# Kernel optimization log

Measured on AMD Instinct MI355X. Metric: run time of the kernel, lower is better.

## Reference

```python
import jax, jax.numpy as jnp
import numpy as np

IN_FEATURES = 4096
OUT_FEATURES = 1024
BATCH = 16384
WERR = 1.0
BERR = 1.0


def setup_inputs() -> dict:
    key = jax.random.key(0)
    kx, kw = jax.random.split(key)
    X = jax.random.normal(kx, (BATCH, IN_FEATURES), dtype=jnp.float32)
    # glorot_uniform init for W, zeros for bias (as in Keras layer)
    limit = np.sqrt(6.0 / (IN_FEATURES + OUT_FEATURES)).astype(np.float32)
    W = jax.random.uniform(kw, (IN_FEATURES, OUT_FEATURES), dtype=jnp.float32,
                           minval=-limit, maxval=limit)
    bias = jnp.zeros((1, OUT_FEATURES), dtype=jnp.float32)
    return {"X": X, "W": W, "bias": bias}


def reference(X, W, bias):
    # Binarize weights/bias with sign(), scaled by Werr/Berr, then dense matmul.
    Wb = jnp.sign(W) * WERR          # [in, out], values in {-1, 0, +1}
    bb = jnp.sign(bias) * BERR       # [1, out]
    Z = jnp.matmul(X, Wb) + bb       # [batch, out]
    return Z
```

## Files before the change

### kernel.cpp

```cpp
#include <hip/hip_runtime.h>

#define M_DIM 16384
#define N_DIM 1024
#define K_DIM 4096

#define BM 256
#define BN 256
#define BK 64
#define NT (K_DIM / BK)

typedef __attribute__((ext_vector_type(4))) float f32x4;
typedef __attribute__((ext_vector_type(8))) short bf16x8;
typedef __attribute__((ext_vector_type(8))) unsigned short u16x8;

static __device__ __forceinline__ short f2bf(float f) {
  union { __bf16 h; short s; } u;
  u.h = (__bf16)f;
  return u.s;
}

static __device__ __forceinline__ void load_lds16(const void* g, void* l) {
  __builtin_amdgcn_global_load_lds(
      (const __attribute__((address_space(1))) void*)g,
      (__attribute__((address_space(3))) void*)l, 16, 0, 0);
}

__global__ __launch_bounds__(256) void wsign_transpose(
    const float* __restrict__ W, unsigned short* __restrict__ WbT) {
  __shared__ unsigned short tile[64][72];
  const int t  = (int)threadIdx.x;
  const int k0 = (int)(blockIdx.x >> 4) * 64;
  const int n0 = (int)(blockIdx.x & 15) * 64;
#pragma unroll
  for (int p = 0; p < 4; ++p) {
    const int r = p * 16 + (t >> 4);
    const int c = (t & 15) * 4;
    const float* src = W + (size_t)(k0 + r) * N_DIM + n0 + c;
#pragma unroll
    for (int j = 0; j < 4; ++j) {
      const float w = src[j];
      tile[r][c + j] = (w > 0.f) ? (unsigned short)0x3F80u
                                 : ((w < 0.f) ? (unsigned short)0xBF80u
                                              : (unsigned short)0u);
    }
  }
  __syncthreads();
  const int n  = t >> 2;
  const int kg = (t & 3) * 16;
  u16x8 o0, o1;
#pragma unroll
  for (int j = 0; j < 8; ++j) o0[j] = tile[kg + j][n];
#pragma unroll
  for (int j = 0; j < 8; ++j) o1[j] = tile[kg + 8 + j][n];
  unsigned short* dst = WbT + (size_t)(n0 + n) * K_DIM + k0 + kg;
  *(u16x8*)dst       = o0;
  *(u16x8*)(dst + 8) = o1;
}

__global__ __launch_bounds__(512, 2) void gemm_kk(
    const float* __restrict__ X, const unsigned short* __restrict__ WbT,
    const float* __restrict__ bias, float* __restrict__ Z) {
  __shared__ __align__(16) unsigned short As[2][BM * BK];
  __shared__ __align__(16) unsigned short Bs[2][BN * BK];

  const int t   = (int)threadIdx.x;
  const int l   = t & 63;
  const int wid = t >> 6;
  const int wm  = wid >> 2;
  const int wn  = wid & 3;

  const int bid = (int)blockIdx.x;
  const int swz = (bid & 7) * 32 + (bid >> 3);
  const int m0  = (swz >> 2) * BM;
  const int n0  = (swz & 3) * BN;

  const int abase = (wm * 128 + (l & 15)) * BK;
  const int bbase = (wn * 64 + (l & 15)) * BK;
  const int axk0  = (((l >> 4) + 0) ^ (l & 7)) << 3;
  const int axk1  = (((l >> 4) + 4) ^ (l & 7)) << 3;

  const float* sA0 = X + (size_t)(m0 +   0 + (t >> 3)) * K_DIM + (t & 7) * 8;
  const float* sA1 = X + (size_t)(m0 +  64 + (t >> 3)) * K_DIM + (t & 7) * 8;
  const float* sA2 = X + (size_t)(m0 + 128 + (t >> 3)) * K_DIM + (t & 7) * 8;
  const float* sA3 = X + (size_t)(m0 + 192 + (t >> 3)) * K_DIM + (t & 7) * 8;
  const int adst = (t >> 3) * BK + (((t & 7) ^ ((t >> 3) & 7)) << 3);

  const unsigned short* b_src[4];
  int b_dst[4];
#pragma unroll
  for (int i = 0; i < 4; ++i) {
    const int c = i * 512 + t;
    const int n = c >> 3, gp = c & 7;
    b_src[i] = WbT + (size_t)(n0 + n) * K_DIM + (gp ^ (n & 7)) * 8;
    b_dst[i] = c * 8;
  }

  f32x4 acc[8][4] = {};
  f32x4 ar[4][2];
  bf16x8 aR[4];
  bf16x8 bR[4];

#define SB0 __builtin_amdgcn_sched_barrier(0)
#define BAR do { SB0; __builtin_amdgcn_s_barrier(); SB0; } while (0)
#define WVM(N) do { asm volatile("s_waitcnt vmcnt(" #N ")" ::: "memory"); SB0; } while (0)
#define WLG0 do { asm volatile("s_waitcnt lgkmcnt(0)" ::: "memory"); SB0; } while (0)

#define LD_A8(KT)                                                          \
  do { SB0;                                                                \
    ar[0][0] = *(const f32x4*)(sA0 + (KT));                                \
    ar[0][1] = *(const f32x4*)(sA0 + (KT) + 4);                            \
    ar[1][0] = *(const f32x4*)(sA1 + (KT));                                \
    ar[1][1] = *(const f32x4*)(sA1 + (KT) + 4);                            \
    ar[2][0] = *(const f32x4*)(sA2 + (KT));                                \
    ar[2][1] = *(const f32x4*)(sA2 + (KT) + 4);                            \
    ar[3][0] = *(const f32x4*)(sA3 + (KT));                                \
    ar[3][1] = *(const f32x4*)(sA3 + (KT) + 4); SB0;                       \
  } while (0)
#define WR_AH(BUF, H)                                                      \
  do {                                                                     \
    _Pragma("unroll") for (int j = 2 * (H); j < 2 * (H) + 2; ++j) {        \
      u16x8 v;                                                             \
      _Pragma("unroll") for (int q = 0; q < 4; ++q) {                      \
        v[q]     = (unsigned short)f2bf(ar[j][0][q]);                      \
        v[4 + q] = (unsigned short)f2bf(ar[j][1][q]);                      \
      }                                                                    \
      *(u16x8*)(&As[BUF][adst + j * 4096]) = v;                            \
    }                                                                      \
  } while (0)
#define DMA_B2(KT, BUF, I0)                                                \
  do { SB0;                                                                \
    _Pragma("unroll") for (int i = (I0); i < (I0) + 2; ++i)                \
      load_lds16(b_src[i] + (KT), &Bs[BUF][b_dst[i]]);                     \
    SB0;                                                                   \
  } while (0)
#define RD_A4(KK, MIG, AB)                                                 \
  do { SB0;                                                                \
    _Pragma("unroll") for (int mi = 0; mi < 4; ++mi)                       \
      aR[mi] = *(const bf16x8*)((AB) + abase + ((MIG)*4 + mi) * 1024 +     \
                                ((KK) ? axk1 : axk0));                     \
    SB0;                                                                   \
  } while (0)
#define RD_B4(KK, BB)                                                      \
  do { SB0;                                                                \
    _Pragma("unroll") for (int nj = 0; nj < 4; ++nj)                       \
      bR[nj] = *(const bf16x8*)((BB) + bbase + nj * 1024 +                 \
                                ((KK) ? axk1 : axk0));                     \
    SB0;                                                                   \
  } while (0)
#define MFMA16(MIG)                                                        \
  do { __builtin_amdgcn_s_setprio(1);                                      \
    _Pragma("unroll") for (int mi = 0; mi < 4; ++mi)                       \
      _Pragma("unroll") for (int nj = 0; nj < 4; ++nj)                     \
        acc[(MIG)*4 + mi][nj] = __builtin_amdgcn_mfma_f32_16x16x32_bf16(   \
            aR[mi], bR[nj], acc[(MIG)*4 + mi][nj], 0, 0, 0);               \
    __builtin_amdgcn_s_setprio(0);                                         \
  } while (0)

  LD_A8(0);
  WVM(0);
  WR_AH(0, 0); WR_AH(0, 1);
  DMA_B2(0, 0, 0); DMA_B2(0, 0, 2);
  LD_A8(BK);
  WVM(8);
  WLG0;
  BAR;

  for (int tt = 0; tt <= NT - 3; ++tt) {
    const int cur = tt & 1, nxt = cur ^ 1;
    const unsigned short* Ab = As[cur];
    const unsigned short* Bb = Bs[cur];
    const int kt1 = (tt + 1) * BK, kt2 = (tt + 2) * BK;
    RD_B4(0, Bb);
    RD_A4(0, 0, Ab);
    DMA_B2(kt1, nxt, 0);
    BAR; WLG0;
    MFMA16(0);
    BAR;
    RD_A4(0, 1, Ab);
    DMA_B2(kt1, nxt, 2);
    WVM(4);
    WR_AH(nxt, 0);
    BAR; WLG0;
    MFMA16(1);
    BAR;
    RD_B4(1, Bb);
    RD_A4(1, 0, Ab);
    WR_AH(nxt, 1);
    LD_A8(kt2);
    BAR; WLG0;
    MFMA16(0);
    BAR;
    RD_A4(1, 1, Ab);
    WVM(8);
    BAR; WLG0;
    MFMA16(1);
    BAR;
  }

  {
    const int cur = (NT - 2) & 1, nxt = cur ^ 1;
    const unsigned short* Ab = As[cur];
    const unsigned short* Bb = Bs[cur];
    const int kt1 = (NT - 1) * BK;
    RD_B4(0, Bb);
    RD_A4(0, 0, Ab);
    DMA_B2(kt1, nxt, 0);
    BAR; WLG0;
    MFMA16(0);
    BAR;
    RD_A4(0, 1, Ab);
    DMA_B2(kt1, nxt, 2);
    WVM(4);
    WR_AH(nxt, 0);
    BAR; WLG0;
    MFMA16(1);
    BAR;
    RD_B4(1, Bb);
    RD_A4(1, 0, Ab);
    WR_AH(nxt, 1);
    BAR; WLG0;
    MFMA16(0);
    BAR;
    RD_A4(1, 1, Ab);
    WVM(0);
    BAR; WLG0;
    MFMA16(1);
    BAR;
  }
  {
    const unsigned short* Ab = As[(NT - 1) & 1];
    const unsigned short* Bb = Bs[(NT - 1) & 1];
    RD_B4(0, Bb);
    RD_A4(0, 0, Ab);
    WLG0;
    MFMA16(0);
    RD_A4(0, 1, Ab);
    WLG0;
    MFMA16(1);
    RD_B4(1, Bb);
    RD_A4(1, 0, Ab);
    WLG0;
    MFMA16(0);
    RD_A4(1, 1, Ab);
    WLG0;
    MFMA16(1);
  }

#pragma unroll
  for (int ni = 0; ni < 4; ++ni) {
    const int col = n0 + wn * 64 + ni * 16 + (l & 15);
    const float b  = bias[col];
    const float bs = (b > 0.f) ? 1.f : ((b < 0.f) ? -1.f : 0.f);
#pragma unroll
    for (int mi = 0; mi < 8; ++mi) {
      const int row = m0 + wm * 128 + mi * 16 + ((l >> 4) << 2);
#pragma unroll
      for (int j = 0; j < 4; ++j)
        Z[(size_t)(row + j) * N_DIM + col] = acc[mi][ni][j] + bs;
    }
  }
#undef SB0
#undef BAR
#undef WVM
#undef WLG0
#undef LD_A8
#undef WR_AH
#undef DMA_B2
#undef RD_A4
#undef RD_B4
#undef MFMA16
}

__global__ __launch_bounds__(256) void naive_fb(
    const float* __restrict__ X, const float* __restrict__ W,
    const float* __restrict__ bias, float* __restrict__ Z) {
  const size_t id = (size_t)blockIdx.x * 256 + threadIdx.x;
  const int m = (int)(id >> 10), n = (int)(id & 1023);
  float acc = 0.f;
  for (int k = 0; k < K_DIM; ++k) {
    const float w = W[(size_t)k * N_DIM + n];
    const float s = (w > 0.f) ? 1.f : ((w < 0.f) ? -1.f : 0.f);
    acc += X[(size_t)m * K_DIM + k] * s;
  }
  const float b = bias[n];
  Z[id] = acc + ((b > 0.f) ? 1.f : ((b < 0.f) ? -1.f : 0.f));
}

extern "C" void kernel_launch(void* const* d_in, const int* in_sizes, int n_in,
                              void* d_out, int out_size, void* d_ws, size_t ws_size,
                              hipStream_t stream) {
  const float* X    = (const float*)d_in[0];
  const float* W    = (const float*)d_in[1];
  const float* bias = (const float*)d_in[2];
  float* Z = (float*)d_out;

  const size_t needW = (size_t)N_DIM * K_DIM * sizeof(unsigned short);
  if (ws_size >= needW) {
    unsigned short* WbT = (unsigned short*)d_ws;
    wsign_transpose<<<dim3((K_DIM / 64) * (N_DIM / 64)), dim3(256), 0, stream>>>(W, WbT);
    gemm_kk<<<dim3((M_DIM / BM) * (N_DIM / BN)), dim3(512), 0, stream>>>(X, WbT, bias, Z);
  } else {
    naive_fb<<<dim3((size_t)M_DIM * N_DIM / 256), dim3(256), 0, stream>>>(X, W, bias, Z);
  }
}
```

Baseline: 177.6 us.

## Double-buffer MFMA register fragments and drop most per-phase barriers in GEMM loop

Rewrites the GEMM main loop to keep two sets of A/B register fragments, so LDS reads for the next MFMA phase overlap with the current phase. Each iteration now uses two workgroup barriers instead of eight, with partial lgkmcnt waits in place of full drains. The four B DMA loads per tile are issued together. Separately, the transpose kernel's LDS tile padding changes to reduce bank conflicts. The cost is more registers and hand-counted wait counts, which could cause races or stalls if any count is wrong.

```diff
diff --git a/kernel.cpp b/kernel.cpp
--- a/kernel.cpp
+++ b/kernel.cpp
@@ -27,7 +27,7 @@
 
 __global__ __launch_bounds__(256) void wsign_transpose(
     const float* __restrict__ W, unsigned short* __restrict__ WbT) {
-  __shared__ unsigned short tile[64][72];
+  __shared__ unsigned short tile[64][67];
   const int t  = (int)threadIdx.x;
   const int k0 = (int)(blockIdx.x >> 4) * 64;
   const int n0 = (int)(blockIdx.x & 15) * 64;
@@ -57,7 +57,7 @@
   *(u16x8*)(dst + 8) = o1;
 }
 
-__global__ __launch_bounds__(512, 2) void gemm_kk(
+__global__ __launch_bounds__(512, 2) void gemm_pipe(
     const float* __restrict__ X, const unsigned short* __restrict__ WbT,
     const float* __restrict__ bias, float* __restrict__ Z) {
   __shared__ __align__(16) unsigned short As[2][BM * BK];
@@ -97,13 +97,13 @@
 
   f32x4 acc[8][4] = {};
   f32x4 ar[4][2];
-  bf16x8 aR[4];
-  bf16x8 bR[4];
+  bf16x8 a0F[4], a1F[4];
+  bf16x8 b0F[4], b1F[4];
 
 #define SB0 __builtin_amdgcn_sched_barrier(0)
 #define BAR do { SB0; __builtin_amdgcn_s_barrier(); SB0; } while (0)
 #define WVM(N) do { asm volatile("s_waitcnt vmcnt(" #N ")" ::: "memory"); SB0; } while (0)
-#define WLG0 do { asm volatile("s_waitcnt lgkmcnt(0)" ::: "memory"); SB0; } while (0)
+#define WLG(N) do { asm volatile("s_waitcnt lgkmcnt(" #N ")" ::: "memory"); SB0; } while (0)
 
 #define LD_A8(KT)                                                          \
   do { SB0;                                                                \
@@ -117,7 +117,7 @@
     ar[3][1] = *(const f32x4*)(sA3 + (KT) + 4); SB0;                       \
   } while (0)
 #define WR_AH(BUF, H)                                                      \
-  do {                                                                     \
+  do { SB0;                                                                \
     _Pragma("unroll") for (int j = 2 * (H); j < 2 * (H) + 2; ++j) {        \
       u16x8 v;                                                             \
       _Pragma("unroll") for (int q = 0; q < 4; ++q) {                      \
@@ -125,75 +125,73 @@
         v[4 + q] = (unsigned short)f2bf(ar[j][1][q]);                      \
       }                                                                    \
       *(u16x8*)(&As[BUF][adst + j * 4096]) = v;                            \
-    }                                                                      \
-  } while (0)
-#define DMA_B2(KT, BUF, I0)                                                \
-  do { SB0;                                                                \
-    _Pragma("unroll") for (int i = (I0); i < (I0) + 2; ++i)                \
+    } SB0;                                                                 \
+  } while (0)
+#define DMA_B4(KT, BUF)                                                    \
+  do { SB0;                                                                \
+    _Pragma("unroll") for (int i = 0; i < 4; ++i)                          \
       load_lds16(b_src[i] + (KT), &Bs[BUF][b_dst[i]]);                     \
     SB0;                                                                   \
   } while (0)
-#define RD_A4(KK, MIG, AB)                                                 \
+#define RD_A(DST, KK, MIG, AB)                                             \
   do { SB0;                                                                \
     _Pragma("unroll") for (int mi = 0; mi < 4; ++mi)                       \
-      aR[mi] = *(const bf16x8*)((AB) + abase + ((MIG)*4 + mi) * 1024 +     \
-                                ((KK) ? axk1 : axk0));                     \
+      DST[mi] = *(const bf16x8*)((AB) + abase + ((MIG)*4 + mi) * 1024 +    \
+                                 ((KK) ? axk1 : axk0));                    \
     SB0;                                                                   \
   } while (0)
-#define RD_B4(KK, BB)                                                      \
+#define RD_B(DST, KK, BB)                                                  \
   do { SB0;                                                                \
     _Pragma("unroll") for (int nj = 0; nj < 4; ++nj)                       \
-      bR[nj] = *(const bf16x8*)((BB) + bbase + nj * 1024 +                 \
-                                ((KK) ? axk1 : axk0));                     \
+      DST[nj] = *(const bf16x8*)((BB) + bbase + nj * 1024 +                \
+                                 ((KK) ? axk1 : axk0));                    \
     SB0;                                                                   \
   } while (0)
-#define MFMA16(MIG)                                                        \
+#define MFMA16(MIG, AF, BF)                                                \
   do { __builtin_amdgcn_s_setprio(1);                                      \
     _Pragma("unroll") for (int mi = 0; mi < 4; ++mi)                       \
       _Pragma("unroll") for (int nj = 0; nj < 4; ++nj)                     \
         acc[(MIG)*4 + mi][nj] = __builtin_amdgcn_mfma_f32_16x16x32_bf16(   \
-            aR[mi], bR[nj], acc[(MIG)*4 + mi][nj], 0, 0, 0);               \
+            AF[mi], BF[nj], acc[(MIG)*4 + mi][nj], 0, 0, 0);               \
     __builtin_amdgcn_s_setprio(0);                                         \
   } while (0)
 
   LD_A8(0);
   WVM(0);
   WR_AH(0, 0); WR_AH(0, 1);
-  DMA_B2(0, 0, 0); DMA_B2(0, 0, 2);
+  DMA_B4(0, 0);
   LD_A8(BK);
   WVM(8);
-  WLG0;
+  WLG(0);
   BAR;
+  RD_A(a0F, 0, 0, As[0]);
+  RD_B(b0F, 0, Bs[0]);
 
   for (int tt = 0; tt <= NT - 3; ++tt) {
     const int cur = tt & 1, nxt = cur ^ 1;
     const unsigned short* Ab = As[cur];
     const unsigned short* Bb = Bs[cur];
-    const int kt1 = (tt + 1) * BK, kt2 = (tt + 2) * BK;
-    RD_B4(0, Bb);
-    RD_A4(0, 0, Ab);
-    DMA_B2(kt1, nxt, 0);
-    BAR; WLG0;
-    MFMA16(0);
-    BAR;
-    RD_A4(0, 1, Ab);
-    DMA_B2(kt1, nxt, 2);
+    RD_A(a1F, 0, 1, Ab);
+    DMA_B4((tt + 1) * BK, nxt);
+    WLG(4);
+    MFMA16(0, a0F, b0F);
+    RD_A(a0F, 1, 0, Ab);
+    RD_B(b1F, 1, Bb);
     WVM(4);
     WR_AH(nxt, 0);
-    BAR; WLG0;
-    MFMA16(1);
-    BAR;
-    RD_B4(1, Bb);
-    RD_A4(1, 0, Ab);
+    WLG(10);
+    MFMA16(1, a1F, b0F);
     WR_AH(nxt, 1);
-    LD_A8(kt2);
-    BAR; WLG0;
-    MFMA16(0);
-    BAR;
-    RD_A4(1, 1, Ab);
+    RD_A(a1F, 1, 1, Ab);
+    LD_A8((tt + 2) * BK);
     WVM(8);
-    BAR; WLG0;
-    MFMA16(1);
+    WLG(4);
+    MFMA16(0, a0F, b1F);
+    BAR;
+    RD_A(a0F, 0, 0, As[nxt]);
+    RD_B(b0F, 0, Bs[nxt]);
+    WLG(8);
+    MFMA16(1, a1F, b1F);
     BAR;
   }
 
@@ -201,49 +199,43 @@
     const int cur = (NT - 2) & 1, nxt = cur ^ 1;
     const unsigned short* Ab = As[cur];
     const unsigned short* Bb = Bs[cur];
-    const int kt1 = (NT - 1) * BK;
-    RD_B4(0, Bb);
-    RD_A4(0, 0, Ab);
-    DMA_B2(kt1, nxt, 0);
-    BAR; WLG0;
-    MFMA16(0);
-    BAR;
-    RD_A4(0, 1, Ab);
-    DMA_B2(kt1, nxt, 2);
+    RD_A(a1F, 0, 1, Ab);
+    DMA_B4((NT - 1) * BK, nxt);
+    WLG(4);
+    MFMA16(0, a0F, b0F);
+    RD_A(a0F, 1, 0, Ab);
+    RD_B(b1F, 1, Bb);
     WVM(4);
     WR_AH(nxt, 0);
-    BAR; WLG0;
-    MFMA16(1);
-    BAR;
-    RD_B4(1, Bb);
-    RD_A4(1, 0, Ab);
+    WLG(10);
+    MFMA16(1, a1F, b0F);
     WR_AH(nxt, 1);
-    BAR; WLG0;
-    MFMA16(0);
-    BAR;
-    RD_A4(1, 1, Ab);
+    RD_A(a1F, 1, 1, Ab);
     WVM(0);
-    BAR; WLG0;
-    MFMA16(1);
+    WLG(4);
+    MFMA16(0, a0F, b1F);
+    BAR;
+    RD_A(a0F, 0, 0, As[nxt]);
+    RD_B(b0F, 0, Bs[nxt]);
+    WLG(8);
+    MFMA16(1, a1F, b1F);
     BAR;
   }
   {
     const unsigned short* Ab = As[(NT - 1) & 1];
     const unsigned short* Bb = Bs[(NT - 1) & 1];
-    RD_B4(0, Bb);
-    RD_A4(0, 0, Ab);
-    WLG0;
-    MFMA16(0);
-    RD_A4(0, 1, Ab);
-    WLG0;
-    MFMA16(1);
-    RD_B4(1, Bb);
-    RD_A4(1, 0, Ab);
-    WLG0;
-    MFMA16(0);
-    RD_A4(1, 1, Ab);
-    WLG0;
-    MFMA16(1);
+    RD_A(a1F, 0, 1, Ab);
+    WLG(4);
+    MFMA16(0, a0F, b0F);
+    RD_A(a0F, 1, 0, Ab);
+    RD_B(b1F, 1, Bb);
+    WLG(8);
+    MFMA16(1, a1F, b0F);
+    RD_A(a1F, 1, 1, Ab);
+    WLG(4);
+    MFMA16(0, a0F, b1F);
+    WLG(0);
+    MFMA16(1, a1F, b1F);
   }
 
 #pragma unroll
@@ -262,12 +254,12 @@
 #undef SB0
 #undef BAR
 #undef WVM
-#undef WLG0
+#undef WLG
 #undef LD_A8
 #undef WR_AH
-#undef DMA_B2
-#undef RD_A4
-#undef RD_B4
+#undef DMA_B4
+#undef RD_A
+#undef RD_B
 #undef MFMA16
 }
 
@@ -298,7 +290,7 @@
   if (ws_size >= needW) {
     unsigned short* WbT = (unsigned short*)d_ws;
     wsign_transpose<<<dim3((K_DIM / 64) * (N_DIM / 64)), dim3(256), 0, stream>>>(W, WbT);
-    gemm_kk<<<dim3((M_DIM / BM) * (N_DIM / BN)), dim3(512), 0, stream>>>(X, WbT, bias, Z);
+    gemm_pipe<<<dim3((M_DIM / BM) * (N_DIM / BN)), dim3(512), 0, stream>>>(X, WbT, bias, Z);
   } else {
     naive_fb<<<dim3((size_t)M_DIM * N_DIM / 256), dim3(256), 0, stream>>>(X, W, bias, Z);
   }
```

Result: faster. 172.2 us (-3.1%).

## Load B fragments directly from global into registers, dropping B LDS staging

Applied to the files above, without the earlier changes.

The GEMM no longer stages the binarized weight tile through LDS with global_load_lds. Each wave now loads its B MFMA fragments straight from global memory into registers, double-buffered across k-halves, which halves LDS usage and removes the B LDS reads. The cost is more redundant global/L2 traffic, since waves sharing a column block each reload B, plus more VGPR pressure from two B register sets. The transpose tile padding also changes from 72 to 67 columns.

```diff
diff --git a/kernel.cpp b/kernel.cpp
--- a/kernel.cpp
+++ b/kernel.cpp
@@ -19,15 +19,9 @@
   return u.s;
 }
 
-static __device__ __forceinline__ void load_lds16(const void* g, void* l) {
-  __builtin_amdgcn_global_load_lds(
-      (const __attribute__((address_space(1))) void*)g,
-      (__attribute__((address_space(3))) void*)l, 16, 0, 0);
-}
-
 __global__ __launch_bounds__(256) void wsign_transpose(
     const float* __restrict__ W, unsigned short* __restrict__ WbT) {
-  __shared__ unsigned short tile[64][72];
+  __shared__ unsigned short tile[64][67];
   const int t  = (int)threadIdx.x;
   const int k0 = (int)(blockIdx.x >> 4) * 64;
   const int n0 = (int)(blockIdx.x & 15) * 64;
@@ -57,11 +51,10 @@
   *(u16x8*)(dst + 8) = o1;
 }
 
-__global__ __launch_bounds__(512, 2) void gemm_kk(
+__global__ __launch_bounds__(512, 2) void gemm_bg(
     const float* __restrict__ X, const unsigned short* __restrict__ WbT,
     const float* __restrict__ bias, float* __restrict__ Z) {
   __shared__ __align__(16) unsigned short As[2][BM * BK];
-  __shared__ __align__(16) unsigned short Bs[2][BN * BK];
 
   const int t   = (int)threadIdx.x;
   const int l   = t & 63;
@@ -75,7 +68,6 @@
   const int n0  = (swz & 3) * BN;
 
   const int abase = (wm * 128 + (l & 15)) * BK;
-  const int bbase = (wn * 64 + (l & 15)) * BK;
   const int axk0  = (((l >> 4) + 0) ^ (l & 7)) << 3;
   const int axk1  = (((l >> 4) + 4) ^ (l & 7)) << 3;
 
@@ -85,28 +77,24 @@
   const float* sA3 = X + (size_t)(m0 + 192 + (t >> 3)) * K_DIM + (t & 7) * 8;
   const int adst = (t >> 3) * BK + (((t & 7) ^ ((t >> 3) & 7)) << 3);
 
-  const unsigned short* b_src[4];
-  int b_dst[4];
-#pragma unroll
-  for (int i = 0; i < 4; ++i) {
-    const int c = i * 512 + t;
-    const int n = c >> 3, gp = c & 7;
-    b_src[i] = WbT + (size_t)(n0 + n) * K_DIM + (gp ^ (n & 7)) * 8;
-    b_dst[i] = c * 8;
-  }
+  const unsigned short* bp[4];
+#pragma unroll
+  for (int nj = 0; nj < 4; ++nj)
+    bp[nj] = WbT + (size_t)(n0 + wn * 64 + nj * 16 + (l & 15)) * K_DIM +
+             (l >> 4) * 8;
 
   f32x4 acc[8][4] = {};
   f32x4 ar[4][2];
-  bf16x8 aR[4];
-  bf16x8 bR[4];
+  bf16x8 aF[4];
+  bf16x8 bB0[4], bB1[4];
 
 #define SB0 __builtin_amdgcn_sched_barrier(0)
 #define BAR do { SB0; __builtin_amdgcn_s_barrier(); SB0; } while (0)
 #define WVM(N) do { asm volatile("s_waitcnt vmcnt(" #N ")" ::: "memory"); SB0; } while (0)
 #define WLG0 do { asm volatile("s_waitcnt lgkmcnt(0)" ::: "memory"); SB0; } while (0)
 
-#define LD_A8(KT)                                                          \
-  do { SB0;                                                                \
+#define LD_AST(KT)                                                         \
+  do {                                                                     \
     ar[0][0] = *(const f32x4*)(sA0 + (KT));                                \
     ar[0][1] = *(const f32x4*)(sA0 + (KT) + 4);                            \
     ar[1][0] = *(const f32x4*)(sA1 + (KT));                                \
@@ -114,11 +102,11 @@
     ar[2][0] = *(const f32x4*)(sA2 + (KT));                                \
     ar[2][1] = *(const f32x4*)(sA2 + (KT) + 4);                            \
     ar[3][0] = *(const f32x4*)(sA3 + (KT));                                \
-    ar[3][1] = *(const f32x4*)(sA3 + (KT) + 4); SB0;                       \
-  } while (0)
-#define WR_AH(BUF, H)                                                      \
-  do {                                                                     \
-    _Pragma("unroll") for (int j = 2 * (H); j < 2 * (H) + 2; ++j) {        \
+    ar[3][1] = *(const f32x4*)(sA3 + (KT) + 4);                            \
+  } while (0)
+#define WR_A(BUF)                                                          \
+  do {                                                                     \
+    _Pragma("unroll") for (int j = 0; j < 4; ++j) {                        \
       u16x8 v;                                                             \
       _Pragma("unroll") for (int q = 0; q < 4; ++q) {                      \
         v[q]     = (unsigned short)f2bf(ar[j][0][q]);                      \
@@ -127,123 +115,102 @@
       *(u16x8*)(&As[BUF][adst + j * 4096]) = v;                            \
     }                                                                      \
   } while (0)
-#define DMA_B2(KT, BUF, I0)                                                \
-  do { SB0;                                                                \
-    _Pragma("unroll") for (int i = (I0); i < (I0) + 2; ++i)                \
-      load_lds16(b_src[i] + (KT), &Bs[BUF][b_dst[i]]);                     \
-    SB0;                                                                   \
+#define LD_B4(SET, KTE)                                                    \
+  do {                                                                     \
+    _Pragma("unroll") for (int nj = 0; nj < 4; ++nj)                       \
+      SET[nj] = *(const bf16x8*)(bp[nj] + (KTE));                          \
   } while (0)
 #define RD_A4(KK, MIG, AB)                                                 \
-  do { SB0;                                                                \
+  do {                                                                     \
     _Pragma("unroll") for (int mi = 0; mi < 4; ++mi)                       \
-      aR[mi] = *(const bf16x8*)((AB) + abase + ((MIG)*4 + mi) * 1024 +     \
+      aF[mi] = *(const bf16x8*)((AB) + abase + ((MIG)*4 + mi) * 1024 +     \
                                 ((KK) ? axk1 : axk0));                     \
-    SB0;                                                                   \
-  } while (0)
-#define RD_B4(KK, BB)                                                      \
-  do { SB0;                                                                \
-    _Pragma("unroll") for (int nj = 0; nj < 4; ++nj)                       \
-      bR[nj] = *(const bf16x8*)((BB) + bbase + nj * 1024 +                 \
-                                ((KK) ? axk1 : axk0));                     \
-    SB0;                                                                   \
-  } while (0)
-#define MFMA16(MIG)                                                        \
+  } while (0)
+#define MFMA16(MIG, BB)                                                    \
   do { __builtin_amdgcn_s_setprio(1);                                      \
     _Pragma("unroll") for (int mi = 0; mi < 4; ++mi)                       \
       _Pragma("unroll") for (int nj = 0; nj < 4; ++nj)                     \
         acc[(MIG)*4 + mi][nj] = __builtin_amdgcn_mfma_f32_16x16x32_bf16(   \
-            aR[mi], bR[nj], acc[(MIG)*4 + mi][nj], 0, 0, 0);               \
+            aF[mi], BB[nj], acc[(MIG)*4 + mi][nj], 0, 0, 0);               \
     __builtin_amdgcn_s_setprio(0);                                         \
   } while (0)
 
-  LD_A8(0);
+  LD_AST(0);
   WVM(0);
-  WR_AH(0, 0); WR_AH(0, 1);
-  DMA_B2(0, 0, 0); DMA_B2(0, 0, 2);
-  LD_A8(BK);
-  WVM(8);
+  WR_A(0);
+  LD_B4(bB0, 0);
+  LD_AST(BK);
   WLG0;
   BAR;
 
   for (int tt = 0; tt <= NT - 3; ++tt) {
     const int cur = tt & 1, nxt = cur ^ 1;
     const unsigned short* Ab = As[cur];
-    const unsigned short* Bb = Bs[cur];
-    const int kt1 = (tt + 1) * BK, kt2 = (tt + 2) * BK;
-    RD_B4(0, Bb);
+    const int kte = tt * BK;
     RD_A4(0, 0, Ab);
-    DMA_B2(kt1, nxt, 0);
-    BAR; WLG0;
-    MFMA16(0);
+    LD_B4(bB1, kte + 32);
+    BAR; WLG0; WVM(12);
+    MFMA16(0, bB0);
     BAR;
     RD_A4(0, 1, Ab);
-    DMA_B2(kt1, nxt, 2);
+    BAR; WLG0;
+    MFMA16(1, bB0);
+    BAR;
+    RD_A4(1, 0, Ab);
     WVM(4);
-    WR_AH(nxt, 0);
-    BAR; WLG0;
-    MFMA16(1);
-    BAR;
-    RD_B4(1, Bb);
-    RD_A4(1, 0, Ab);
-    WR_AH(nxt, 1);
-    LD_A8(kt2);
-    BAR; WLG0;
-    MFMA16(0);
+    WR_A(nxt);
+    LD_B4(bB0, kte + BK);
+    LD_AST(kte + 2 * BK);
+    BAR; WLG0; WVM(12);
+    MFMA16(0, bB1);
     BAR;
     RD_A4(1, 1, Ab);
-    WVM(8);
-    BAR; WLG0;
-    MFMA16(1);
+    BAR; WLG0;
+    MFMA16(1, bB1);
     BAR;
   }
 
   {
     const int cur = (NT - 2) & 1, nxt = cur ^ 1;
     const unsigned short* Ab = As[cur];
-    const unsigned short* Bb = Bs[cur];
-    const int kt1 = (NT - 1) * BK;
-    RD_B4(0, Bb);
+    const int kte = (NT - 2) * BK;
     RD_A4(0, 0, Ab);
-    DMA_B2(kt1, nxt, 0);
-    BAR; WLG0;
-    MFMA16(0);
+    LD_B4(bB1, kte + 32);
+    BAR; WLG0; WVM(12);
+    MFMA16(0, bB0);
     BAR;
     RD_A4(0, 1, Ab);
-    DMA_B2(kt1, nxt, 2);
+    BAR; WLG0;
+    MFMA16(1, bB0);
+    BAR;
+    RD_A4(1, 0, Ab);
     WVM(4);
-    WR_AH(nxt, 0);
-    BAR; WLG0;
-    MFMA16(1);
-    BAR;
-    RD_B4(1, Bb);
-    RD_A4(1, 0, Ab);
-    WR_AH(nxt, 1);
-    BAR; WLG0;
-    MFMA16(0);
+    WR_A(nxt);
+    LD_B4(bB0, kte + BK);
+    BAR; WLG0; WVM(4);
+    MFMA16(0, bB1);
     BAR;
     RD_A4(1, 1, Ab);
-    WVM(0);
-    BAR; WLG0;
-    MFMA16(1);
+    BAR; WLG0;
+    MFMA16(1, bB1);
     BAR;
   }
   {
     const unsigned short* Ab = As[(NT - 1) & 1];
-    const unsigned short* Bb = Bs[(NT - 1) & 1];
-    RD_B4(0, Bb);
+    const int kte = (NT - 1) * BK;
     RD_A4(0, 0, Ab);
-    WLG0;
-    MFMA16(0);
+    LD_B4(bB1, kte + 32);
+    WLG0; WVM(4);
+    MFMA16(0, bB0);
     RD_A4(0, 1, Ab);
     WLG0;
-    MFMA16(1);
-    RD_B4(1, Bb);
+    MFMA16(1, bB0);
     RD_A4(1, 0, Ab);
-    WLG0;
-    MFMA16(0);
+    WLG0; WVM(0);
+    MFMA16(0, bB1);
     RD_A4(1, 1, Ab);
     WLG0;
-    MFMA16(1);
+    MFMA16(1, bB1);
   }
 
 #pragma unroll
@@ -263,11 +230,10 @@
 #undef BAR
 #undef WVM
 #undef WLG0
-#undef LD_A8
-#undef WR_AH
-#undef DMA_B2
+#undef LD_AST
+#undef WR_A
+#undef LD_B4
 #undef RD_A4
-#undef RD_B4
 #undef MFMA16
 }
 
@@ -298,7 +264,7 @@
   if (ws_size >= needW) {
     unsigned short* WbT = (unsigned short*)d_ws;
     wsign_transpose<<<dim3((K_DIM / 64) * (N_DIM / 64)), dim3(256), 0, stream>>>(W, WbT);
-    gemm_kk<<<dim3((M_DIM / BM) * (N_DIM / BN)), dim3(512), 0, stream>>>(X, WbT, bias, Z);
+    gemm_bg<<<dim3((M_DIM / BM) * (N_DIM / BN)), dim3(512), 0, stream>>>(X, WbT, bias, Z);
   } else {
     naive_fb<<<dim3((size_t)M_DIM * N_DIM / 256), dim3(256), 0, stream>>>(X, W, bias, Z);
   }
```

After: 211.5 us. 1.19x slower.

## Restructure A-tile staging into even/odd row halves and reorder MFMA phases

Applied to the files above, without the earlier changes.

Changes how X rows are loaded and converted to bf16. Each thread now loads 16 contiguous floats for two rows (an even and an odd 64-row group) and writes them into a new LDS layout of four 64-row quadrants. The main loop is reordered to run k-half-major with two B register sets (bR0, bR1). A-tile global loads and bf16 writes are split across phases, including an early write into the current buffer after its reads finish, to spread the conversion work and memory waits more evenly. The cost is extra B registers and a more delicate vmcnt and barrier ordering, which could cause hazards or register pressure.

```diff
diff --git a/kernel.cpp b/kernel.cpp
--- a/kernel.cpp
+++ b/kernel.cpp
@@ -57,10 +57,10 @@
   *(u16x8*)(dst + 8) = o1;
 }
 
-__global__ __launch_bounds__(512, 2) void gemm_kk(
+__global__ __launch_bounds__(512, 2) void gemm_ks(
     const float* __restrict__ X, const unsigned short* __restrict__ WbT,
     const float* __restrict__ bias, float* __restrict__ Z) {
-  __shared__ __align__(16) unsigned short As[2][BM * BK];
+  __shared__ __align__(16) unsigned short As[2][4 * 4096];
   __shared__ __align__(16) unsigned short Bs[2][BN * BK];
 
   const int t   = (int)threadIdx.x;
@@ -74,16 +74,19 @@
   const int m0  = (swz >> 2) * BM;
   const int n0  = (swz & 3) * BN;
 
-  const int abase = (wm * 128 + (l & 15)) * BK;
+  const int arow  = (l & 15) * 64;
   const int bbase = (wn * 64 + (l & 15)) * BK;
   const int axk0  = (((l >> 4) + 0) ^ (l & 7)) << 3;
   const int axk1  = (((l >> 4) + 4) ^ (l & 7)) << 3;
 
-  const float* sA0 = X + (size_t)(m0 +   0 + (t >> 3)) * K_DIM + (t & 7) * 8;
-  const float* sA1 = X + (size_t)(m0 +  64 + (t >> 3)) * K_DIM + (t & 7) * 8;
-  const float* sA2 = X + (size_t)(m0 + 128 + (t >> 3)) * K_DIM + (t & 7) * 8;
-  const float* sA3 = X + (size_t)(m0 + 192 + (t >> 3)) * K_DIM + (t & 7) * 8;
-  const int adst = (t >> 3) * BK + (((t & 7) ^ ((t >> 3) & 7)) << 3);
+  const int wr_row = t >> 2, jj = t & 3;
+  const int inner  = wr_row & 63;
+  const int hi     = wr_row >> 6;
+  const int rowE   = hi ? (128 + inner) : inner;
+  const float* srcE = X + (size_t)(m0 + rowE) * K_DIM + jj * 16;
+  const float* srcO = srcE + (size_t)64 * K_DIM;
+  const int dstE0 = (hi ? 2 : 0) * 4096 + inner * 64 + (((2 * jj) ^ (inner & 7)) << 3);
+  const int dstE1 = (hi ? 2 : 0) * 4096 + inner * 64 + (((2 * jj + 1) ^ (inner & 7)) << 3);
 
   const unsigned short* b_src[4];
   int b_dst[4];
@@ -96,36 +99,40 @@
   }
 
   f32x4 acc[8][4] = {};
-  f32x4 ar[4][2];
+  f32x4 arE[4], arO[4];
   bf16x8 aR[4];
-  bf16x8 bR[4];
+  bf16x8 bR0[4], bR1[4];
 
 #define SB0 __builtin_amdgcn_sched_barrier(0)
 #define BAR do { SB0; __builtin_amdgcn_s_barrier(); SB0; } while (0)
 #define WVM(N) do { asm volatile("s_waitcnt vmcnt(" #N ")" ::: "memory"); SB0; } while (0)
 #define WLG0 do { asm volatile("s_waitcnt lgkmcnt(0)" ::: "memory"); SB0; } while (0)
 
-#define LD_A8(KT)                                                          \
-  do { SB0;                                                                \
-    ar[0][0] = *(const f32x4*)(sA0 + (KT));                                \
-    ar[0][1] = *(const f32x4*)(sA0 + (KT) + 4);                            \
-    ar[1][0] = *(const f32x4*)(sA1 + (KT));                                \
-    ar[1][1] = *(const f32x4*)(sA1 + (KT) + 4);                            \
-    ar[2][0] = *(const f32x4*)(sA2 + (KT));                                \
-    ar[2][1] = *(const f32x4*)(sA2 + (KT) + 4);                            \
-    ar[3][0] = *(const f32x4*)(sA3 + (KT));                                \
-    ar[3][1] = *(const f32x4*)(sA3 + (KT) + 4); SB0;                       \
-  } while (0)
-#define WR_AH(BUF, H)                                                      \
+#define LD_ARE(KT)                                                         \
+  do { SB0;                                                                \
+    arE[0] = *(const f32x4*)(srcE + (KT));                                 \
+    arE[1] = *(const f32x4*)(srcE + (KT) + 4);                             \
+    arE[2] = *(const f32x4*)(srcE + (KT) + 8);                             \
+    arE[3] = *(const f32x4*)(srcE + (KT) + 12); SB0;                       \
+  } while (0)
+#define LD_ARO(KT)                                                         \
+  do { SB0;                                                                \
+    arO[0] = *(const f32x4*)(srcO + (KT));                                 \
+    arO[1] = *(const f32x4*)(srcO + (KT) + 4);                             \
+    arO[2] = *(const f32x4*)(srcO + (KT) + 8);                             \
+    arO[3] = *(const f32x4*)(srcO + (KT) + 12); SB0;                       \
+  } while (0)
+#define WR_AR(AR, BUF, QOFS)                                               \
   do {                                                                     \
-    _Pragma("unroll") for (int j = 2 * (H); j < 2 * (H) + 2; ++j) {        \
-      u16x8 v;                                                             \
-      _Pragma("unroll") for (int q = 0; q < 4; ++q) {                      \
-        v[q]     = (unsigned short)f2bf(ar[j][0][q]);                      \
-        v[4 + q] = (unsigned short)f2bf(ar[j][1][q]);                      \
-      }                                                                    \
-      *(u16x8*)(&As[BUF][adst + j * 4096]) = v;                            \
+    u16x8 v0, v1;                                                          \
+    _Pragma("unroll") for (int q = 0; q < 4; ++q) {                        \
+      v0[q]     = (unsigned short)f2bf(AR[0][q]);                          \
+      v0[4 + q] = (unsigned short)f2bf(AR[1][q]);                          \
+      v1[q]     = (unsigned short)f2bf(AR[2][q]);                          \
+      v1[4 + q] = (unsigned short)f2bf(AR[3][q]);                          \
     }                                                                      \
+    *(u16x8*)(&As[BUF][dstE0 + (QOFS)]) = v0;                              \
+    *(u16x8*)(&As[BUF][dstE1 + (QOFS)]) = v1;                              \
   } while (0)
 #define DMA_B2(KT, BUF, I0)                                                \
   do { SB0;                                                                \
@@ -133,35 +140,37 @@
       load_lds16(b_src[i] + (KT), &Bs[BUF][b_dst[i]]);                     \
     SB0;                                                                   \
   } while (0)
-#define RD_A4(KK, MIG, AB)                                                 \
+#define RD_A(MIG, KK, AB)                                                  \
   do { SB0;                                                                \
     _Pragma("unroll") for (int mi = 0; mi < 4; ++mi)                       \
-      aR[mi] = *(const bf16x8*)((AB) + abase + ((MIG)*4 + mi) * 1024 +     \
-                                ((KK) ? axk1 : axk0));                     \
+      aR[mi] = *(const bf16x8*)((AB) + (wm * 2 + (MIG)) * 4096 + arow +    \
+                                mi * 1024 + ((KK) ? axk1 : axk0));         \
     SB0;                                                                   \
   } while (0)
-#define RD_B4(KK, BB)                                                      \
+#define RD_B(SET, KK, BB)                                                  \
   do { SB0;                                                                \
     _Pragma("unroll") for (int nj = 0; nj < 4; ++nj)                       \
-      bR[nj] = *(const bf16x8*)((BB) + bbase + nj * 1024 +                 \
-                                ((KK) ? axk1 : axk0));                     \
+      SET[nj] = *(const bf16x8*)((BB) + bbase + nj * 1024 +                \
+                                 ((KK) ? axk1 : axk0));                    \
     SB0;                                                                   \
   } while (0)
-#define MFMA16(MIG)                                                        \
+#define MFMA16(MIG, BSET)                                                  \
   do { __builtin_amdgcn_s_setprio(1);                                      \
     _Pragma("unroll") for (int mi = 0; mi < 4; ++mi)                       \
       _Pragma("unroll") for (int nj = 0; nj < 4; ++nj)                     \
         acc[(MIG)*4 + mi][nj] = __builtin_amdgcn_mfma_f32_16x16x32_bf16(   \
-            aR[mi], bR[nj], acc[(MIG)*4 + mi][nj], 0, 0, 0);               \
+            aR[mi], BSET[nj], acc[(MIG)*4 + mi][nj], 0, 0, 0);             \
     __builtin_amdgcn_s_setprio(0);                                         \
   } while (0)
 
-  LD_A8(0);
+  LD_ARE(0); LD_ARO(0);
   WVM(0);
-  WR_AH(0, 0); WR_AH(0, 1);
+  WR_AR(arE, 0, 0); WR_AR(arO, 0, 4096);
   DMA_B2(0, 0, 0); DMA_B2(0, 0, 2);
-  LD_A8(BK);
-  WVM(8);
+  LD_ARE(BK);
+  WVM(0);
+  WR_AR(arE, 1, 0);
+  LD_ARO(BK);
   WLG0;
   BAR;
 
@@ -170,30 +179,32 @@
     const unsigned short* Ab = As[cur];
     const unsigned short* Bb = Bs[cur];
     const int kt1 = (tt + 1) * BK, kt2 = (tt + 2) * BK;
-    RD_B4(0, Bb);
-    RD_A4(0, 0, Ab);
+    RD_A(0, 0, Ab);
+    RD_B(bR0, 0, Bb);
+    LD_ARE(kt2);
     DMA_B2(kt1, nxt, 0);
-    BAR; WLG0;
-    MFMA16(0);
-    BAR;
-    RD_A4(0, 1, Ab);
+    WVM(6);
+    WR_AR(arO, nxt, 4096);
+    BAR; WLG0;
+    MFMA16(0, bR0);
+    BAR;
+    RD_A(0, 1, Ab);
+    RD_B(bR1, 1, Bb);
+    LD_ARO(kt2);
     DMA_B2(kt1, nxt, 2);
+    BAR; WLG0;
+    MFMA16(0, bR1);
+    BAR;
+    RD_A(1, 0, Ab);
+    WVM(8);
+    WR_AR(arE, cur, 0);
+    BAR; WLG0;
+    MFMA16(1, bR0);
+    BAR;
+    RD_A(1, 1, Ab);
     WVM(4);
-    WR_AH(nxt, 0);
-    BAR; WLG0;
-    MFMA16(1);
-    BAR;
-    RD_B4(1, Bb);
-    RD_A4(1, 0, Ab);
-    WR_AH(nxt, 1);
-    LD_A8(kt2);
-    BAR; WLG0;
-    MFMA16(0);
-    BAR;
-    RD_A4(1, 1, Ab);
-    WVM(8);
-    BAR; WLG0;
-    MFMA16(1);
+    BAR; WLG0;
+    MFMA16(1, bR1);
     BAR;
   }
 
@@ -202,48 +213,47 @@
     const unsigned short* Ab = As[cur];
     const unsigned short* Bb = Bs[cur];
     const int kt1 = (NT - 1) * BK;
-    RD_B4(0, Bb);
-    RD_A4(0, 0, Ab);
+    RD_A(0, 0, Ab);
+    RD_B(bR0, 0, Bb);
     DMA_B2(kt1, nxt, 0);
-    BAR; WLG0;
-    MFMA16(0);
-    BAR;
-    RD_A4(0, 1, Ab);
+    WVM(2);
+    WR_AR(arO, nxt, 4096);
+    BAR; WLG0;
+    MFMA16(0, bR0);
+    BAR;
+    RD_A(0, 1, Ab);
+    RD_B(bR1, 1, Bb);
     DMA_B2(kt1, nxt, 2);
-    WVM(4);
-    WR_AH(nxt, 0);
-    BAR; WLG0;
-    MFMA16(1);
-    BAR;
-    RD_B4(1, Bb);
-    RD_A4(1, 0, Ab);
-    WR_AH(nxt, 1);
-    BAR; WLG0;
-    MFMA16(0);
-    BAR;
-    RD_A4(1, 1, Ab);
+    BAR; WLG0;
+    MFMA16(0, bR1);
+    BAR;
+    RD_A(1, 0, Ab);
+    BAR; WLG0;
+    MFMA16(1, bR0);
+    BAR;
+    RD_A(1, 1, Ab);
     WVM(0);
     BAR; WLG0;
-    MFMA16(1);
+    MFMA16(1, bR1);
     BAR;
   }
   {
     const unsigned short* Ab = As[(NT - 1) & 1];
     const unsigned short* Bb = Bs[(NT - 1) & 1];
-    RD_B4(0, Bb);
-    RD_A4(0, 0, Ab);
+    RD_A(0, 0, Ab);
+    RD_B(bR0, 0, Bb);
     WLG0;
-    MFMA16(0);
-    RD_A4(0, 1, Ab);
+    MFMA16(0, bR0);
+    RD_A(0, 1, Ab);
+    RD_B(bR1, 1, Bb);
     WLG0;
-    MFMA16(1);
-    RD_B4(1, Bb);
-    RD_A4(1, 0, Ab);
+    MFMA16(0, bR1);
+    RD_A(1, 0, Ab);
     WLG0;
-    MFMA16(0);
-    RD_A4(1, 1, Ab);
+    MFMA16(1, bR0);
+    RD_A(1, 1, Ab);
     WLG0;
-    MFMA16(1);
+    MFMA16(1, bR1);
   }
 
 #pragma unroll
@@ -263,11 +273,12 @@
 #undef BAR
 #undef WVM
 #undef WLG0
-#undef LD_A8
-#undef WR_AH
+#undef LD_ARE
+#undef LD_ARO
+#undef WR_AR
 #undef DMA_B2
-#undef RD_A4
-#undef RD_B4
+#undef RD_A
+#undef RD_B
 #undef MFMA16
 }
 
@@ -298,7 +309,7 @@
   if (ws_size >= needW) {
     unsigned short* WbT = (unsigned short*)d_ws;
     wsign_transpose<<<dim3((K_DIM / 64) * (N_DIM / 64)), dim3(256), 0, stream>>>(W, WbT);
-    gemm_kk<<<dim3((M_DIM / BM) * (N_DIM / BN)), dim3(512), 0, stream>>>(X, WbT, bias, Z);
+    gemm_ks<<<dim3((M_DIM / BM) * (N_DIM / BN)), dim3(512), 0, stream>>>(X, WbT, bias, Z);
   } else {
     naive_fb<<<dim3((size_t)M_DIM * N_DIM / 256), dim3(256), 0, stream>>>(X, W, bias, Z);
   }
```

Measured after the change: 242.2 us. +36.4%, slower.
